# Optimization experiments

Measured on AMD Instinct MI355X. Metric: run time of the kernel, lower is better.

## Reference

```python
import jax, jax.numpy as jnp
import numpy as np

LORA_RANK = 16
LORA_ALPHA = 32.0
LORA_SCALE = LORA_ALPHA / LORA_RANK
W_BITS = 8
A_BITS = 8


def fake_quant(x, bits):
    """Symmetric per-tensor fake quantization with straight-through estimator."""
    qmax = 2.0 ** (bits - 1) - 1.0
    scale = jnp.maximum(jnp.max(jnp.abs(x)), 1e-8) / qmax
    q = jnp.clip(jnp.round(x / scale), -qmax, qmax) * scale
    return x + jax.lax.stop_gradient(q - x)  # STE


def quant_linear_lora(x, W, b, A, B):
    # x: [..., in], W: [out, in], A: [r, in], B: [out, r]
    xq = fake_quant(x, A_BITS)
    Wq = fake_quant(W, W_BITS)
    base = jnp.einsum('bsi,oi->bso', xq, Wq) + b
    lora = jnp.einsum('bsr,or->bso', jnp.einsum('bsi,ri->bsr', x, A), B)
    return base + LORA_SCALE * lora


def setup_inputs() -> dict:
    key = jax.random.key(0)
    ks = jax.random.split(key, 9)
    n_embd, d_ff, B_, S = 1024, 4096, 4, 2048
    s_in = 1.0 / np.sqrt(n_embd)
    s_ff = 1.0 / np.sqrt(d_ff)
    return {
        'hidden_states': jax.random.normal(ks[0], (B_, S, n_embd), jnp.float32),
        'W_fc': jax.random.normal(ks[1], (d_ff, n_embd), jnp.float32) * s_in,
        'b_fc': jax.random.normal(ks[2], (d_ff,), jnp.float32) * 0.02,
        'A_fc': jax.random.normal(ks[3], (LORA_RANK, n_embd), jnp.float32) * s_in,
        'B_fc': jax.random.normal(ks[4], (d_ff, LORA_RANK), jnp.float32) * 0.01,
        'W_proj': jax.random.normal(ks[5], (n_embd, d_ff), jnp.float32) * s_ff,
        'b_proj': jax.random.normal(ks[6], (n_embd,), jnp.float32) * 0.02,
        'A_proj': jax.random.normal(ks[7], (LORA_RANK, d_ff), jnp.float32) * s_ff,
        'B_proj': jax.random.normal(ks[8], (n_embd, LORA_RANK), jnp.float32) * 0.01,
    }


def reference(hidden_states, W_fc, b_fc, A_fc, B_fc, W_proj, b_proj, A_proj, B_proj):
    h = quant_linear_lora(hidden_states, W_fc, b_fc, A_fc, B_fc)
    h = jax.nn.gelu(h, approximate=False)  # nn.GELU() default = exact erf GELU
    h = quant_linear_lora(h, W_proj, b_proj, A_proj, B_proj)
    return h
```

## Files before the change

kernel.cpp:

```cpp
#include <hip/hip_runtime.h>
#include <stdint.h>

using i32x4 = __attribute__((ext_vector_type(4))) int;
using f32x4 = __attribute__((ext_vector_type(4))) float;
using f16x4 = __attribute__((ext_vector_type(4))) _Float16;

#define M_TOK 8192
#define N_EMB 1024
#define D_FF  4096

__device__ __forceinline__ void async_lds16(void* lds, const void* g) {
  __builtin_amdgcn_global_load_lds(
      (const __attribute__((address_space(1))) void*)g,
      (__attribute__((address_space(3))) void*)lds, 16, 0, 0);
}

__global__ void zero_slots_k(unsigned* s) {
  if (threadIdx.x < 16) s[threadIdx.x] = 0u;
}

__global__ void absmax_k(const float* __restrict__ p, long n, unsigned* __restrict__ slot) {
  long i = ((long)blockIdx.x * blockDim.x + threadIdx.x) * 4;
  long stride = (long)gridDim.x * blockDim.x * 4;
  float m = 0.f;
  for (; i < n; i += stride) {
    float4 v = *(const float4*)(p + i);
    m = fmaxf(m, fmaxf(fmaxf(fabsf(v.x), fabsf(v.y)), fmaxf(fabsf(v.z), fabsf(v.w))));
  }
  for (int o = 32; o; o >>= 1) m = fmaxf(m, __shfl_xor(m, o));
  __shared__ float sm[4];
  if ((threadIdx.x & 63) == 0) sm[threadIdx.x >> 6] = m;
  __syncthreads();
  if (threadIdx.x == 0) {
    m = fmaxf(fmaxf(sm[0], sm[1]), fmaxf(sm[2], sm[3]));
    atomicMax(slot, __float_as_uint(m));
  }
}

__global__ void quant_k(const float* __restrict__ p, int8_t* __restrict__ q, long n,
                        const unsigned* __restrict__ slot) {
  float inv = 127.f / fmaxf(__uint_as_float(*slot), 1e-8f);
  long i = ((long)blockIdx.x * blockDim.x + threadIdx.x) * 4;
  long stride = (long)gridDim.x * blockDim.x * 4;
  for (; i < n; i += stride) {
    float4 v = *(const float4*)(p + i);
    int b0 = (int)fminf(fmaxf(rintf(v.x * inv), -127.f), 127.f);
    int b1 = (int)fminf(fmaxf(rintf(v.y * inv), -127.f), 127.f);
    int b2 = (int)fminf(fmaxf(rintf(v.z * inv), -127.f), 127.f);
    int b3 = (int)fminf(fmaxf(rintf(v.w * inv), -127.f), 127.f);
    int w = (b0 & 0xff) | ((b1 & 0xff) << 8) | ((b2 & 0xff) << 16) | ((b3 & 0xff) << 24);
    *(int*)(q + i) = w;
  }
}

__global__ void prep_bfrag_k(const float* __restrict__ A, _Float16* __restrict__ Bp, int K) {
  int s = blockIdx.x;
  int l = threadIdx.x;
  int r = l & 15, g = l >> 4;
  float4 v = *(const float4*)(A + (long)r * K + s * 16 + g * 4);
  f16x4 h;
  h[0] = (_Float16)v.x; h[1] = (_Float16)v.y; h[2] = (_Float16)v.z; h[3] = (_Float16)v.w;
  *(f16x4*)(Bp + ((long)s * 64 + l) * 4) = h;
}

__global__ __launch_bounds__(512) void lora_quant_k(
    const float* __restrict__ X, const _Float16* __restrict__ Bpre,
    const unsigned* __restrict__ slot, int8_t* __restrict__ Q,
    float* __restrict__ T, int K) {
  int lane = threadIdx.x & 63, wave = threadIdx.x >> 6;
  int row0 = blockIdx.x * 16;
  int r = lane & 15, g = lane >> 4;
  float inv = 127.f / fmaxf(__uint_as_float(*slot), 1e-8f);

  int kPerWave = K >> 3;
  int kbase = wave * kPerWave;
  const float* xrow = X + (long)(row0 + r) * K;
  int8_t* qrow = Q + (long)(row0 + r) * K;

  f32x4 acc = {0.f, 0.f, 0.f, 0.f};
  int nsteps = kPerWave >> 4;
#pragma unroll 4
  for (int s = 0; s < nsteps; s++) {
    int k = kbase + s * 16 + g * 4;
    float4 v = *(const float4*)(xrow + k);
    int b0 = (int)fminf(fmaxf(rintf(v.x * inv), -127.f), 127.f);
    int b1 = (int)fminf(fmaxf(rintf(v.y * inv), -127.f), 127.f);
    int b2 = (int)fminf(fmaxf(rintf(v.z * inv), -127.f), 127.f);
    int b3 = (int)fminf(fmaxf(rintf(v.w * inv), -127.f), 127.f);
    *(int*)(qrow + k) = (b0 & 0xff) | ((b1 & 0xff) << 8) | ((b2 & 0xff) << 16) | ((b3 & 0xff) << 24);
    f16x4 a;
    a[0] = (_Float16)v.x; a[1] = (_Float16)v.y; a[2] = (_Float16)v.z; a[3] = (_Float16)v.w;
    int gs = (kbase + s * 16) >> 4;
    f16x4 b = *(const f16x4*)(Bpre + ((long)gs * 64 + lane) * 4);
    acc = __builtin_amdgcn_mfma_f32_16x16x16f16(a, b, acc, 0, 0, 0);
  }

  __shared__ float part[8][16][17];
#pragma unroll
  for (int j = 0; j < 4; j++) part[wave][g * 4 + j][r] = acc[j];
  __syncthreads();
  int t = threadIdx.x;
  if (t < 256) {
    int m = t >> 4, rr = t & 15;
    float sum = 0.f;
#pragma unroll
    for (int w = 0; w < 8; w++) sum += part[w][m][rr];
    T[(long)(row0 + m) * 16 + rr] = 2.0f * sum;
  }
}

template <bool GELU>
__global__ __launch_bounds__(256, 3) void gemm_q8(
    const int8_t* __restrict__ Aq, const int8_t* __restrict__ Bq,
    int M, int N, int K,
    const unsigned* __restrict__ sa, const unsigned* __restrict__ sb,
    const float* __restrict__ bias,
    const float* __restrict__ T,
    const float* __restrict__ Bl,
    float* __restrict__ C, unsigned* hmax) {
  __shared__ __align__(16) int8_t As[16384];
  __shared__ __align__(16) int8_t Bs[16384];

  int bn = blockIdx.x * 128;
  int bm = blockIdx.y * 128;

  int t = threadIdx.x;
  int lane = t & 63, wave = t >> 6;
  int wr = wave >> 1, wc = wave & 1;
  int l16 = lane & 15, lq = lane >> 4;

  int ldst[4];
  const int8_t* srcA[4];
  const int8_t* srcB[4];
#pragma unroll
  for (int i = 0; i < 4; i++) {
    int s = i * 256 + t;
    int row = s >> 3;
    int cg = (s & 7) ^ (row & 7);
    ldst[i] = s * 16;
    srcA[i] = Aq + (long)(bm + row) * K + cg * 16;
    srcB[i] = Bq + (long)(bn + row) * K + cg * 16;
  }

  int aoff[4], boff[4];
#pragma unroll
  for (int mf = 0; mf < 4; mf++) {
    int row = wr * 64 + mf * 16 + l16;
    aoff[mf] = row * 128 + ((lq ^ (row & 7)) << 4);
  }
#pragma unroll
  for (int nf = 0; nf < 4; nf++) {
    int row = wc * 64 + nf * 16 + l16;
    boff[nf] = row * 128 + ((lq ^ (row & 7)) << 4);
  }

  i32x4 acc[4][4] = {};
  int KT = K >> 7;

  for (int kt = 0; kt < KT; ++kt) {
    long ko = (long)kt * 128;
#pragma unroll
    for (int i = 0; i < 4; i++) async_lds16(As + ldst[i], srcA[i] + ko);
#pragma unroll
    for (int i = 0; i < 4; i++) async_lds16(Bs + ldst[i], srcB[i] + ko);
    __syncthreads();

#pragma unroll
    for (int kh = 0; kh < 2; kh++) {
      int kx = kh << 6;
      i32x4 av[4], bv[4];
#pragma unroll
      for (int mf = 0; mf < 4; mf++) av[mf] = *(const i32x4*)(As + (aoff[mf] ^ kx));
#pragma unroll
      for (int nf = 0; nf < 4; nf++) bv[nf] = *(const i32x4*)(Bs + (boff[nf] ^ kx));
#pragma unroll
      for (int mf = 0; mf < 4; mf++)
#pragma unroll
        for (int nf = 0; nf < 4; nf++)
          acc[mf][nf] = __builtin_amdgcn_mfma_i32_16x16x64_i8(av[mf], bv[nf], acc[mf][nf], 0, 0, 0);
    }
    __syncthreads();
  }

  float s = (fmaxf(__uint_as_float(*sa), 1e-8f) * (1.f / 127.f)) *
            (fmaxf(__uint_as_float(*sb), 1e-8f) * (1.f / 127.f));

  f16x4 af[4], bf[4];
#pragma unroll
  for (int mf = 0; mf < 4; mf++) {
    int m = bm + wr * 64 + mf * 16 + l16;
    float4 tv = *(const float4*)(T + (long)m * 16 + lq * 4);
    f16x4 v; v[0] = (_Float16)tv.x; v[1] = (_Float16)tv.y; v[2] = (_Float16)tv.z; v[3] = (_Float16)tv.w;
    af[mf] = v;
  }
#pragma unroll
  for (int nf = 0; nf < 4; nf++) {
    int n = bn + wc * 64 + nf * 16 + l16;
    float4 bv4 = *(const float4*)(Bl + (long)n * 16 + lq * 4);
    f16x4 v; v[0] = (_Float16)bv4.x; v[1] = (_Float16)bv4.y; v[2] = (_Float16)bv4.z; v[3] = (_Float16)bv4.w;
    bf[nf] = v;
  }
  float bias_v[4];
#pragma unroll
  for (int nf = 0; nf < 4; nf++) bias_v[nf] = bias[bn + wc * 64 + nf * 16 + l16];

  float lmax = 0.f;
#pragma unroll
  for (int mf = 0; mf < 4; mf++) {
#pragma unroll
    for (int nf = 0; nf < 4; nf++) {
      f32x4 fa = __builtin_amdgcn_mfma_f32_16x16x16f16(af[mf], bf[nf], f32x4{0.f, 0.f, 0.f, 0.f}, 0, 0, 0);
      int n = bn + wc * 64 + nf * 16 + l16;
#pragma unroll
      for (int j = 0; j < 4; j++) {
        int m = bm + wr * 64 + mf * 16 + lq * 4 + j;
        float v = s * (float)acc[mf][nf][j] + bias_v[nf] + fa[j];
        if constexpr (GELU) {
          v = 0.5f * v * (1.0f + erff(v * 0.70710678118654752f));
          lmax = fmaxf(lmax, fabsf(v));
        }
        C[(long)m * N + n] = v;
      }
    }
  }
  if constexpr (GELU) {
    for (int o = 32; o; o >>= 1) lmax = fmaxf(lmax, __shfl_xor(lmax, o));
    if (lane == 0) atomicMax(hmax, __float_as_uint(lmax));
  }
}

extern "C" void kernel_launch(void* const* d_in, const int* in_sizes, int n_in,
                              void* d_out, int out_size, void* d_ws, size_t ws_size,
                              hipStream_t stream) {
  const float* x   = (const float*)d_in[0];
  const float* Wfc = (const float*)d_in[1];
  const float* bfc = (const float*)d_in[2];
  const float* Afc = (const float*)d_in[3];
  const float* Bfc = (const float*)d_in[4];
  const float* Wpj = (const float*)d_in[5];
  const float* bpj = (const float*)d_in[6];
  const float* Apj = (const float*)d_in[7];
  const float* Bpj = (const float*)d_in[8];
  float* out = (float*)d_out;

  char* ws = (char*)d_ws;
  unsigned* slots = (unsigned*)ws;
  int8_t* qx  = (int8_t*)(ws + 256);
  int8_t* qwf = qx  + (size_t)M_TOK * N_EMB;
  int8_t* qwp = qwf + (size_t)D_FF * N_EMB;
  int8_t* qh  = qwp + (size_t)N_EMB * D_FF;
  float*  t1  = (float*)(qh + (size_t)M_TOK * D_FF);
  float*  t2  = t1  + (size_t)M_TOK * 16;
  _Float16* Bp1 = (_Float16*)(t2 + (size_t)M_TOK * 16);
  _Float16* Bp2 = Bp1 + (size_t)N_EMB * 16;
  float*  h   = (float*)(Bp2 + (size_t)D_FF * 16);

  zero_slots_k<<<1, 64, 0, stream>>>(slots);
  absmax_k<<<1024, 256, 0, stream>>>(x,   (long)M_TOK * N_EMB, slots + 0);
  absmax_k<<<1024, 256, 0, stream>>>(Wfc, (long)D_FF * N_EMB,  slots + 1);
  absmax_k<<<1024, 256, 0, stream>>>(Wpj, (long)N_EMB * D_FF,  slots + 2);

  quant_k<<<2048, 256, 0, stream>>>(Wfc, qwf, (long)D_FF * N_EMB, slots + 1);
  quant_k<<<2048, 256, 0, stream>>>(Wpj, qwp, (long)N_EMB * D_FF, slots + 2);

  prep_bfrag_k<<<N_EMB / 16, 64, 0, stream>>>(Afc, Bp1, N_EMB);
  prep_bfrag_k<<<D_FF / 16, 64, 0, stream>>>(Apj, Bp2, D_FF);

  lora_quant_k<<<M_TOK / 16, 512, 0, stream>>>(x, Bp1, slots + 0, qx, t1, N_EMB);

  gemm_q8<true><<<dim3(D_FF / 128, M_TOK / 128), 256, 0, stream>>>(
      qx, qwf, M_TOK, D_FF, N_EMB, slots + 0, slots + 1, bfc, t1, Bfc, h, slots + 3);

  lora_quant_k<<<M_TOK / 16, 512, 0, stream>>>(h, Bp2, slots + 3, qh, t2, D_FF);

  gemm_q8<false><<<dim3(N_EMB / 128, M_TOK / 128), 256, 0, stream>>>(
      qh, qwp, M_TOK, N_EMB, D_FF, slots + 3, slots + 2, bpj, t2, Bpj, out, nullptr);
}
```

Baseline: 303.0 us.

## Double-buffer int8 GEMM with larger tiles, 512 threads and XCD-aware block remap

Replaces the single-buffered 128x128 int8 GEMM with a 256xBN tile kernel using 8 waves. The A and B tiles are double-buffered in LDS with manual vmcnt waits, so global loads for the next K step overlap the MFMA work, and s_setprio raises priority around the MFMA loop. Block IDs are remapped across the 8 XCDs to improve L2 locality. It uses more LDS and registers, which may lower occupancy, and the hand-written waitcnt and barrier sequence is fragile.

```diff
diff --git a/kernel.cpp b/kernel.cpp
--- a/kernel.cpp
+++ b/kernel.cpp
@@ -109,111 +109,153 @@
   }
 }
 
-template <bool GELU>
-__global__ __launch_bounds__(256, 3) void gemm_q8(
+template <bool GELU, int NF>
+__global__ __launch_bounds__(512, 2) void gemm8p(
     const int8_t* __restrict__ Aq, const int8_t* __restrict__ Bq,
-    int M, int N, int K,
+    int N, int K,
     const unsigned* __restrict__ sa, const unsigned* __restrict__ sb,
     const float* __restrict__ bias,
     const float* __restrict__ T,
     const float* __restrict__ Bl,
     float* __restrict__ C, unsigned* hmax) {
-  __shared__ __align__(16) int8_t As[16384];
-  __shared__ __align__(16) int8_t Bs[16384];
-
-  int bn = blockIdx.x * 128;
-  int bm = blockIdx.y * 128;
+  constexpr int BN = NF * 64;
+  constexpr int BBUF = BN * 128;
+  __shared__ __align__(16) int8_t lds[65536 + 2 * BBUF];
+  int8_t* ldsA = lds;
+  int8_t* ldsB = lds + 65536;
+
+  int nwg = gridDim.x * gridDim.y;
+  int lid = blockIdx.y * gridDim.x + blockIdx.x;
+  int cpx = nwg >> 3;
+  int nid = (lid & 7) * cpx + (lid >> 3);
+  int bn = (nid % gridDim.x) * BN;
+  int bm = (nid / gridDim.x) * 256;
 
   int t = threadIdx.x;
   int lane = t & 63, wave = t >> 6;
-  int wr = wave >> 1, wc = wave & 1;
+  int wr = wave >> 2, wc = wave & 3;
   int l16 = lane & 15, lq = lane >> 4;
 
-  int ldst[4];
-  const int8_t* srcA[4];
-  const int8_t* srcB[4];
+  const int8_t* gA = Aq + (long)bm * K;
+  const int8_t* gB = Bq + (long)bn * K;
+
+  int aDst[4], aSrc[4];
 #pragma unroll
   for (int i = 0; i < 4; i++) {
-    int s = i * 256 + t;
-    int row = s >> 3;
-    int cg = (s & 7) ^ (row & 7);
-    ldst[i] = s * 16;
-    srcA[i] = Aq + (long)(bm + row) * K + cg * 16;
-    srcB[i] = Bq + (long)(bn + row) * K + cg * 16;
-  }
-
-  int aoff[4], boff[4];
-#pragma unroll
-  for (int mf = 0; mf < 4; mf++) {
-    int row = wr * 64 + mf * 16 + l16;
+    int s = i * 512 + t, row = s >> 3;
+    aDst[i] = s * 16;
+    aSrc[i] = row * K + (((s & 7) ^ (row & 7)) << 4);
+  }
+  int bDst[NF], bSrc[NF];
+#pragma unroll
+  for (int i = 0; i < NF; i++) {
+    int s = i * 512 + t, row = s >> 3;
+    bDst[i] = s * 16;
+    bSrc[i] = row * K + (((s & 7) ^ (row & 7)) << 4);
+  }
+
+  int aoff[8], boff[NF];
+#pragma unroll
+  for (int mf = 0; mf < 8; mf++) {
+    int row = wr * 128 + mf * 16 + l16;
     aoff[mf] = row * 128 + ((lq ^ (row & 7)) << 4);
   }
 #pragma unroll
-  for (int nf = 0; nf < 4; nf++) {
-    int row = wc * 64 + nf * 16 + l16;
+  for (int nf = 0; nf < NF; nf++) {
+    int row = wc * (NF * 16) + nf * 16 + l16;
     boff[nf] = row * 128 + ((lq ^ (row & 7)) << 4);
   }
 
-  i32x4 acc[4][4] = {};
+  i32x4 acc[8][NF] = {};
   int KT = K >> 7;
 
+#pragma unroll
+  for (int i = 0; i < 4; i++) async_lds16(ldsA + aDst[i], gA + aSrc[i]);
+#pragma unroll
+  for (int i = 0; i < NF; i++) async_lds16(ldsB + bDst[i], gB + bSrc[i]);
+#pragma unroll
+  for (int i = 0; i < 4; i++) async_lds16(ldsA + 32768 + aDst[i], gA + aSrc[i] + 128);
+  asm volatile("s_waitcnt vmcnt(4)" ::: "memory");
+  __builtin_amdgcn_s_barrier();
+  __builtin_amdgcn_sched_barrier(0);
+
   for (int kt = 0; kt < KT; ++kt) {
-    long ko = (long)kt * 128;
-#pragma unroll
-    for (int i = 0; i < 4; i++) async_lds16(As + ldst[i], srcA[i] + ko);
-#pragma unroll
-    for (int i = 0; i < 4; i++) async_lds16(Bs + ldst[i], srcB[i] + ko);
-    __syncthreads();
-
-#pragma unroll
-    for (int kh = 0; kh < 2; kh++) {
-      int kx = kh << 6;
-      i32x4 av[4], bv[4];
-#pragma unroll
-      for (int mf = 0; mf < 4; mf++) av[mf] = *(const i32x4*)(As + (aoff[mf] ^ kx));
-#pragma unroll
-      for (int nf = 0; nf < 4; nf++) bv[nf] = *(const i32x4*)(Bs + (boff[nf] ^ kx));
-#pragma unroll
-      for (int mf = 0; mf < 4; mf++)
-#pragma unroll
-        for (int nf = 0; nf < 4; nf++)
+    const int8_t* Ab = ldsA + (kt & 1) * 32768;
+    const int8_t* Bb = ldsB + (kt & 1) * BBUF;
+
+    if (kt + 1 < KT) {
+      long ko = (long)(kt + 1) * 128;
+      int nb = ((kt + 1) & 1) * BBUF;
+#pragma unroll
+      for (int i = 0; i < NF; i++) async_lds16(ldsB + nb + bDst[i], gB + bSrc[i] + ko);
+    }
+
+#pragma unroll
+    for (int ks = 0; ks < 2; ks++) {
+      int kx = ks << 6;
+      i32x4 av[8], bv[NF];
+#pragma unroll
+      for (int mf = 0; mf < 8; mf++) av[mf] = *(const i32x4*)(Ab + (aoff[mf] ^ kx));
+#pragma unroll
+      for (int nf = 0; nf < NF; nf++) bv[nf] = *(const i32x4*)(Bb + (boff[nf] ^ kx));
+      __builtin_amdgcn_s_setprio(1);
+#pragma unroll
+      for (int mf = 0; mf < 8; mf++)
+#pragma unroll
+        for (int nf = 0; nf < NF; nf++)
           acc[mf][nf] = __builtin_amdgcn_mfma_i32_16x16x64_i8(av[mf], bv[nf], acc[mf][nf], 0, 0, 0);
+      __builtin_amdgcn_s_setprio(0);
     }
-    __syncthreads();
+
+    __builtin_amdgcn_sched_barrier(0);
+    __builtin_amdgcn_s_barrier();
+    if (kt + 2 < KT) {
+      long ko = (long)(kt + 2) * 128;
+      int nb = (kt & 1) * 32768;
+#pragma unroll
+      for (int i = 0; i < 4; i++) async_lds16(ldsA + nb + aDst[i], gA + aSrc[i] + ko);
+      asm volatile("s_waitcnt vmcnt(4)" ::: "memory");
+      __builtin_amdgcn_s_barrier();
+      __builtin_amdgcn_sched_barrier(0);
+    } else if (kt + 1 < KT) {
+      asm volatile("s_waitcnt vmcnt(0)" ::: "memory");
+      __builtin_amdgcn_s_barrier();
+      __builtin_amdgcn_sched_barrier(0);
+    }
   }
 
   float s = (fmaxf(__uint_as_float(*sa), 1e-8f) * (1.f / 127.f)) *
             (fmaxf(__uint_as_float(*sb), 1e-8f) * (1.f / 127.f));
 
-  f16x4 af[4], bf[4];
-#pragma unroll
-  for (int mf = 0; mf < 4; mf++) {
-    int m = bm + wr * 64 + mf * 16 + l16;
+  f16x4 af[8], bf[NF];
+#pragma unroll
+  for (int mf = 0; mf < 8; mf++) {
+    int m = bm + wr * 128 + mf * 16 + l16;
     float4 tv = *(const float4*)(T + (long)m * 16 + lq * 4);
     f16x4 v; v[0] = (_Float16)tv.x; v[1] = (_Float16)tv.y; v[2] = (_Float16)tv.z; v[3] = (_Float16)tv.w;
     af[mf] = v;
   }
 #pragma unroll
-  for (int nf = 0; nf < 4; nf++) {
-    int n = bn + wc * 64 + nf * 16 + l16;
+  for (int nf = 0; nf < NF; nf++) {
+    int n = bn + wc * (NF * 16) + nf * 16 + l16;
     float4 bv4 = *(const float4*)(Bl + (long)n * 16 + lq * 4);
     f16x4 v; v[0] = (_Float16)bv4.x; v[1] = (_Float16)bv4.y; v[2] = (_Float16)bv4.z; v[3] = (_Float16)bv4.w;
     bf[nf] = v;
   }
-  float bias_v[4];
-#pragma unroll
-  for (int nf = 0; nf < 4; nf++) bias_v[nf] = bias[bn + wc * 64 + nf * 16 + l16];
+  float bias_v[NF];
+#pragma unroll
+  for (int nf = 0; nf < NF; nf++) bias_v[nf] = bias[bn + wc * (NF * 16) + nf * 16 + l16];
 
   float lmax = 0.f;
 #pragma unroll
-  for (int mf = 0; mf < 4; mf++) {
-#pragma unroll
-    for (int nf = 0; nf < 4; nf++) {
+  for (int mf = 0; mf < 8; mf++) {
+#pragma unroll
+    for (int nf = 0; nf < NF; nf++) {
       f32x4 fa = __builtin_amdgcn_mfma_f32_16x16x16f16(af[mf], bf[nf], f32x4{0.f, 0.f, 0.f, 0.f}, 0, 0, 0);
-      int n = bn + wc * 64 + nf * 16 + l16;
+      int n = bn + wc * (NF * 16) + nf * 16 + l16;
 #pragma unroll
       for (int j = 0; j < 4; j++) {
-        int m = bm + wr * 64 + mf * 16 + lq * 4 + j;
+        int m = bm + wr * 128 + mf * 16 + lq * 4 + j;
         float v = s * (float)acc[mf][nf][j] + bias_v[nf] + fa[j];
         if constexpr (GELU) {
           v = 0.5f * v * (1.0f + erff(v * 0.70710678118654752f));
@@ -268,11 +310,11 @@
 
   lora_quant_k<<<M_TOK / 16, 512, 0, stream>>>(x, Bp1, slots + 0, qx, t1, N_EMB);
 
-  gemm_q8<true><<<dim3(D_FF / 128, M_TOK / 128), 256, 0, stream>>>(
-      qx, qwf, M_TOK, D_FF, N_EMB, slots + 0, slots + 1, bfc, t1, Bfc, h, slots + 3);
+  gemm8p<true, 4><<<dim3(D_FF / 256, M_TOK / 256), 512, 0, stream>>>(
+      qx, qwf, D_FF, N_EMB, slots + 0, slots + 1, bfc, t1, Bfc, h, slots + 3);
 
   lora_quant_k<<<M_TOK / 16, 512, 0, stream>>>(h, Bp2, slots + 3, qh, t2, D_FF);
 
-  gemm_q8<false><<<dim3(N_EMB / 128, M_TOK / 128), 256, 0, stream>>>(
-      qh, qwp, M_TOK, N_EMB, D_FF, slots + 3, slots + 2, bpj, t2, Bpj, out, nullptr);
-}
+  gemm8p<false, 2><<<dim3(N_EMB / 128, M_TOK / 256), 512, 0, stream>>>(
+      qh, qwp, N_EMB, D_FF, slots + 3, slots + 2, bpj, t2, Bpj, out, nullptr);
+}
```

After: 280.2 us. 1.08x faster.
